# Optimization experiments

Hardware: AMD Instinct MI355X
Metric: run time of the kernel (lower is better)

The kernel has to match this reference:

```python
import jax, jax.numpy as jnp
import numpy as np

DIM = 512
HEADS = 8
HEAD_DIM = DIM // HEADS
SCALE = HEAD_DIM ** -0.5


def setup_inputs() -> dict:
    key = jax.random.key(0)
    ks = jax.random.split(key, 9)
    B, N, C = 4, 256, DIM
    w = lambda k, shape: jax.random.normal(k, shape, dtype=jnp.float32) * (shape[-1] ** -0.5)
    return {
        "q": jax.random.normal(ks[0], (B, N, C), dtype=jnp.float32),
        "k": jax.random.normal(ks[1], (B, N, C), dtype=jnp.float32),
        "v": jax.random.normal(ks[2], (B, N, C), dtype=jnp.float32),
        "relation_feature": jax.random.normal(ks[3], (B, N, N, C), dtype=jnp.float32),
        "W_q": w(ks[4], (C, C)),      # torch Linear weight: y = x @ W.T
        "W_k": w(ks[5], (C, C)),
        "W_v": w(ks[6], (C, C)),
        "W_r_conv": w(ks[7], (HEADS, C)),
        "W_r_qk": w(ks[8], (2 * C, C)),
    }


def reference(q, k, v, relation_feature, W_q, W_k, W_v, W_r_conv, W_r_qk):
    B, N1, C = q.shape
    N2 = k.shape[1]
    H, HS = HEADS, HEAD_DIM

    # project and split heads -> [B, H, N, HS]
    qh = (q @ W_q.T).reshape(B, N1, H, HS).transpose(0, 2, 1, 3)
    kh = (k @ W_k.T).reshape(B, N2, H, HS).transpose(0, 2, 1, 3)
    vh = (v @ W_v.T).reshape(B, N2, H, HS).transpose(0, 2, 1, 3)

    attn_J = jnp.einsum("bhnd,bhmd->bhnm", qh, kh)  # [B,H,N1,N2]

    # Relation-conditioned projections (computed in the original forward but
    # unused in the returned output; kept here for faithfulness of the math).
    R_qkv = (relation_feature @ W_r_qk.T).reshape(B, N1, N2, 2, H, HS)
    R_q = R_qkv[:, :, :, 0].transpose(0, 3, 1, 2, 4)  # [B,H,N1,N2,HS]
    R_k = R_qkv[:, :, :, 1].transpose(0, 3, 1, 2, 4)
    attn_R_qurt = jnp.einsum("bhnmd,bhnmd->bhnm", R_q, R_k)  # unused
    attn_R_linear = jnp.einsum("bnmc,hc->bhnm", relation_feature, W_r_conv)  # unused
    del attn_R_qurt, attn_R_linear

    attn = jax.nn.softmax(attn_J * SCALE, axis=-1)  # dropout p=0 -> identity
    x = jnp.einsum("bhnm,bhmd->bhnd", attn, vh).transpose(0, 2, 1, 3).reshape(B, N1, C)
    return (x, attn)
```

## Files before the change

kernel.cpp:

```cpp
#include <hip/hip_runtime.h>

#define HEADS 8
#define HD 64
#define NN 256
#define CC 512
#define SCALE 0.125f
#define NBLK 384
#define MAGICV 0x5F3A9C71u

typedef _Float16 half4v __attribute__((ext_vector_type(4)));
typedef _Float16 half8v __attribute__((ext_vector_type(8)));
typedef float f32x4 __attribute__((ext_vector_type(4)));

static __device__ __forceinline__ void st_agent(void* p, half4v v) {
    union { half4v h; unsigned long long u; } c;
    c.h = v;
    __hip_atomic_store((unsigned long long*)p, c.u, __ATOMIC_RELAXED,
                       __HIP_MEMORY_SCOPE_AGENT);
}

__global__ __launch_bounds__(256, 2) void fused_kernel(
    const float* __restrict__ q, const float* __restrict__ k,
    const float* __restrict__ v, const float* __restrict__ Wq,
    const float* __restrict__ Wk, const float* __restrict__ Wv,
    _Float16* __restrict__ qh, _Float16* __restrict__ kh,
    _Float16* __restrict__ vT, float* __restrict__ attn,
    float* __restrict__ x, unsigned* __restrict__ flag)
{
    __shared__ __align__(16) char smem[26624];

    const int t = threadIdx.x;
    const int lane = t & 63;
    const int blk = blockIdx.x;

    {
        _Float16 (*Xs)[72] = (_Float16 (*)[72])smem;
        _Float16 (*Ws)[72] = (_Float16 (*)[72])(smem + 9216);
        const int w = t >> 6;
        const int wr = w >> 1, wc = w & 1;
        const int l15 = lane & 15, g = lane >> 4;
        const int sc = t & 7, sr = t >> 3;

        const int z = blk >> 7;
        const int rem = blk & 127;
        const int r0 = (rem >> 3) * 64;
        const int c0 = (rem & 7) * 64;
        const float* __restrict__ X = (z == 0) ? q : (z == 1) ? k : v;
        const float* __restrict__ W = (z == 0) ? Wq : (z == 1) ? Wk : Wv;

        f32x4 acc[2][2] = {};

        for (int k0 = 0; k0 < CC; k0 += 64) {
            #pragma unroll
            for (int p = 0; p < 2; ++p) {
                int row = sr + p * 32;
                const float* gx = X + (r0 + row) * CC + k0 + sc * 8;
                const float* gw = W + (c0 + row) * CC + k0 + sc * 8;
                float4 x0 = *(const float4*)gx, x1 = *(const float4*)(gx + 4);
                float4 w0 = *(const float4*)gw, w1 = *(const float4*)(gw + 4);
                half8v hx, hw;
                hx[0] = (_Float16)x0.x; hx[1] = (_Float16)x0.y;
                hx[2] = (_Float16)x0.z; hx[3] = (_Float16)x0.w;
                hx[4] = (_Float16)x1.x; hx[5] = (_Float16)x1.y;
                hx[6] = (_Float16)x1.z; hx[7] = (_Float16)x1.w;
                hw[0] = (_Float16)w0.x; hw[1] = (_Float16)w0.y;
                hw[2] = (_Float16)w0.z; hw[3] = (_Float16)w0.w;
                hw[4] = (_Float16)w1.x; hw[5] = (_Float16)w1.y;
                hw[6] = (_Float16)w1.z; hw[7] = (_Float16)w1.w;
                *(half8v*)&Xs[row][sc * 8] = hx;
                *(half8v*)&Ws[row][sc * 8] = hw;
            }
            __syncthreads();
            #pragma unroll
            for (int kk = 0; kk < 2; ++kk) {
                half8v af[2], bf[2];
                #pragma unroll
                for (int mi = 0; mi < 2; ++mi)
                    af[mi] = *(const half8v*)((z == 2)
                        ? &Xs[wr * 32 + mi * 16 + l15][kk * 32 + g * 8]
                        : &Ws[wr * 32 + mi * 16 + l15][kk * 32 + g * 8]);
                #pragma unroll
                for (int ni = 0; ni < 2; ++ni)
                    bf[ni] = *(const half8v*)((z == 2)
                        ? &Ws[wc * 32 + ni * 16 + l15][kk * 32 + g * 8]
                        : &Xs[wc * 32 + ni * 16 + l15][kk * 32 + g * 8]);
                #pragma unroll
                for (int mi = 0; mi < 2; ++mi)
                    #pragma unroll
                    for (int ni = 0; ni < 2; ++ni)
                        acc[mi][ni] = __builtin_amdgcn_mfma_f32_16x16x32_f16(
                            af[mi], bf[ni], acc[mi][ni], 0, 0, 0);
            }
            __syncthreads();
        }

        #pragma unroll
        for (int mi = 0; mi < 2; ++mi) {
            #pragma unroll
            for (int ni = 0; ni < 2; ++ni) {
                f32x4 a = acc[mi][ni];
                half4v hv;
                hv[0] = (_Float16)a[0]; hv[1] = (_Float16)a[1];
                hv[2] = (_Float16)a[2]; hv[3] = (_Float16)a[3];
                if (z < 2) {
                    int ch  = c0 + wr * 32 + mi * 16 + g * 4;
                    int tok = r0 + wc * 32 + ni * 16 + l15;
                    int bb = tok >> 8, n = tok & 255, h = ch >> 6, d = ch & 63;
                    _Float16* dst = ((z == 0) ? qh : kh)
                                  + (((bb * HEADS + h) * NN + n) * HD + d);
                    st_agent(dst, hv);
                } else {
                    int tok = r0 + wr * 32 + mi * 16 + g * 4;
                    int ch  = c0 + wc * 32 + ni * 16 + l15;
                    int bb = tok >> 8, m = tok & 255, h = ch >> 6, d = ch & 63;
                    _Float16* dst = vT + (((bb * HEADS + h) * HD + d) * NN + m);
                    st_agent(dst, hv);
                }
            }
        }
    }

    __syncthreads();
    if (t == 0)
        __hip_atomic_store(flag + blk, MAGICV, __ATOMIC_RELAXED,
                           __HIP_MEMORY_SCOPE_AGENT);
    if (blk >= 256) return;

    {
        const int bbb = blk >> 6;
        const int hh  = (blk >> 3) & 7;
        const int nt  = blk & 7;
        if (t < 9) {
            int dep;
            if (t == 0)      dep = (bbb * 4 + (nt >> 1)) * 8 + hh;
            else if (t < 5)  dep = 128 + (bbb * 4 + (t - 1)) * 8 + hh;
            else             dep = 256 + (bbb * 4 + (t - 5)) * 8 + hh;
            while (__hip_atomic_load(flag + dep, __ATOMIC_RELAXED,
                                     __HIP_MEMORY_SCOPE_AGENT) != MAGICV)
                __builtin_amdgcn_s_sleep(2);
        }
        __syncthreads();
    }

    const int bh = blk >> 3, bb = bh >> 3, h = bh & 7;
    const int n0 = (blk & 7) * 32;
    const int w = __builtin_amdgcn_readfirstlane(t >> 6);
    const int rg = w & 1, mh = w >> 1;
    const int l15 = lane & 15, g = lane >> 4;
    const int n = n0 + rg * 16 + l15;

    _Float16 (*Plds)[16][136] = (_Float16 (*)[16][136])smem;
    float* red  = (float*)(smem + 17408);
    float* Olds = (float*)(smem + 17920);

    const _Float16* qb = qh + (bh * NN + n) * HD + g * 8;
    half8v bq0 = *(const half8v*)qb;
    half8v bq1 = *(const half8v*)(qb + 32);

    f32x4 acc[8] = {};
    const _Float16* kb = kh + (bh * NN + mh * 128 + l15) * HD + g * 8;
    #pragma unroll
    for (int nf = 0; nf < 8; ++nf) {
        half8v a0 = *(const half8v*)(kb + nf * 16 * HD);
        half8v a1 = *(const half8v*)(kb + nf * 16 * HD + 32);
        acc[nf] = __builtin_amdgcn_mfma_f32_16x16x32_f16(a0, bq0, acc[nf], 0, 0, 0);
        acc[nf] = __builtin_amdgcn_mfma_f32_16x16x32_f16(a1, bq1, acc[nf], 0, 0, 0);
    }

    float mx = -3.0e38f;
    #pragma unroll
    for (int nf = 0; nf < 8; ++nf)
        #pragma unroll
        for (int r = 0; r < 4; ++r) mx = fmaxf(mx, acc[nf][r]);
    mx = fmaxf(mx, __shfl_xor(mx, 16, 64));
    mx = fmaxf(mx, __shfl_xor(mx, 32, 64));
    const float ml = mx * SCALE;

    float sloc = 0.f;
    #pragma unroll
    for (int nf = 0; nf < 8; ++nf)
        #pragma unroll
        for (int r = 0; r < 4; ++r) {
            float e = __expf(acc[nf][r] * SCALE - ml);
            acc[nf][r] = e;
            sloc += e;
        }
    sloc += __shfl_xor(sloc, 16, 64);
    sloc += __shfl_xor(sloc, 32, 64);

    if (g == 0) {
        red[((rg * 2 + mh) * 16 + l15) * 2 + 0] = ml;
        red[((rg * 2 + mh) * 16 + l15) * 2 + 1] = sloc;
    }
    __syncthreads();
    const float mo = red[((rg * 2 + (mh ^ 1)) * 16 + l15) * 2 + 0];
    const float so = red[((rg * 2 + (mh ^ 1)) * 16 + l15) * 2 + 1];
    const float M = fmaxf(ml, mo);
    const float fl = __expf(ml - M);
    const float pscale = fl / (sloc * fl + so * __expf(mo - M));

    float* arow = attn + (bh * NN + n) * NN + mh * 128;
    #pragma unroll
    for (int nf = 0; nf < 8; ++nf) {
        float4 pv4;
        pv4.x = acc[nf][0] * pscale; pv4.y = acc[nf][1] * pscale;
        pv4.z = acc[nf][2] * pscale; pv4.w = acc[nf][3] * pscale;
        *(float4*)(arow + nf * 16 + g * 4) = pv4;
        half4v hv;
        hv[0] = (_Float16)pv4.x; hv[1] = (_Float16)pv4.y;
        hv[2] = (_Float16)pv4.z; hv[3] = (_Float16)pv4.w;
        *(half4v*)&Plds[w][l15][nf * 16 + g * 4] = hv;
    }
    asm volatile("s_waitcnt lgkmcnt(0)" ::: "memory");

    half8v pb[4];
    #pragma unroll
    for (int mt = 0; mt < 4; ++mt)
        pb[mt] = *(const half8v*)&Plds[w][l15][mt * 32 + g * 8];

    f32x4 O[4] = {};
    #pragma unroll
    for (int df = 0; df < 4; ++df) {
        const _Float16* vb = vT + (bh * HD + df * 16 + l15) * NN + mh * 128 + g * 8;
        #pragma unroll
        for (int mt = 0; mt < 4; ++mt) {
            half8v av = *(const half8v*)(vb + mt * 32);
            O[df] = __builtin_amdgcn_mfma_f32_16x16x32_f16(av, pb[mt], O[df], 0, 0, 0);
        }
    }

    if (mh == 1) {
        #pragma unroll
        for (int df = 0; df < 4; ++df)
            *(f32x4*)&Olds[(rg * 16 + l15) * 68 + df * 16 + g * 4] = O[df];
    }
    __syncthreads();
    if (mh == 0) {
        float* xb = x + (bb * NN + n) * CC + h * HD;
        #pragma unroll
        for (int df = 0; df < 4; ++df) {
            f32x4 o2 = *(const f32x4*)&Olds[(rg * 16 + l15) * 68 + df * 16 + g * 4];
            float4 st;
            st.x = O[df][0] + o2[0]; st.y = O[df][1] + o2[1];
            st.z = O[df][2] + o2[2]; st.w = O[df][3] + o2[3];
            *(float4*)(xb + df * 16 + g * 4) = st;
        }
    }
}

extern "C" void kernel_launch(void* const* d_in, const int* in_sizes, int n_in,
                              void* d_out, int out_size, void* d_ws, size_t ws_size,
                              hipStream_t stream) {
    const float* q  = (const float*)d_in[0];
    const float* k  = (const float*)d_in[1];
    const float* v  = (const float*)d_in[2];
    const float* Wq = (const float*)d_in[4];
    const float* Wk = (const float*)d_in[5];
    const float* Wv = (const float*)d_in[6];

    float* x    = (float*)d_out;
    float* attn = (float*)d_out + 4 * 256 * 512;

    _Float16* qh = (_Float16*)d_ws;
    _Float16* kh = qh + 32 * 256 * 64;
    _Float16* vT = kh + 32 * 256 * 64;
    unsigned* flag = (unsigned*)((char*)d_ws + (4u << 20));

    fused_kernel<<<dim3(NBLK), dim3(256), 0, stream>>>(
        q, k, v, Wq, Wk, Wv, qh, kh, vT, attn, x, flag);
}
```

Baseline: 25.71 us.

## Stage full B operand in LDS once and stream A fragments from global

The projection phase now loads the whole 64x512 B-operand tile into shared memory in a single pass, then removes the per-k-step LDS staging and barriers. Each wave reads its A-operand fragments straight from global memory into registers, converting to fp16 inline, with the k loop fully unrolled. The aim is to drop the 16 __syncthreads per tile and the LDS round trip for A. In exchange, LDS use grows to about 65 KB, which may reduce the 2-blocks-per-CU occupancy, and A is reloaded from global by the two waves that share a row band.

```diff
diff --git a/kernel.cpp b/kernel.cpp
--- a/kernel.cpp
+++ b/kernel.cpp
@@ -11,6 +11,15 @@
 typedef _Float16 half4v __attribute__((ext_vector_type(4)));
 typedef _Float16 half8v __attribute__((ext_vector_type(8)));
 typedef float f32x4 __attribute__((ext_vector_type(4)));
+
+static __device__ __forceinline__ half8v cvt8(float4 a, float4 b) {
+    half8v h;
+    h[0] = (_Float16)a.x; h[1] = (_Float16)a.y;
+    h[2] = (_Float16)a.z; h[3] = (_Float16)a.w;
+    h[4] = (_Float16)b.x; h[5] = (_Float16)b.y;
+    h[6] = (_Float16)b.z; h[7] = (_Float16)b.w;
+    return h;
+}
 
 static __device__ __forceinline__ void st_agent(void* p, half4v v) {
     union { half4v h; unsigned long long u; } c;
@@ -27,19 +36,17 @@
     _Float16* __restrict__ vT, float* __restrict__ attn,
     float* __restrict__ x, unsigned* __restrict__ flag)
 {
-    __shared__ __align__(16) char smem[26624];
+    __shared__ __align__(16) char smem[66560];
 
     const int t = threadIdx.x;
     const int lane = t & 63;
     const int blk = blockIdx.x;
 
     {
-        _Float16 (*Xs)[72] = (_Float16 (*)[72])smem;
-        _Float16 (*Ws)[72] = (_Float16 (*)[72])(smem + 9216);
+        _Float16 (*Bs)[520] = (_Float16 (*)[520])smem;
         const int w = t >> 6;
         const int wr = w >> 1, wc = w & 1;
         const int l15 = lane & 15, g = lane >> 4;
-        const int sc = t & 7, sr = t >> 3;
 
         const int z = blk >> 7;
         const int rem = blk & 127;
@@ -48,50 +55,48 @@
         const float* __restrict__ X = (z == 0) ? q : (z == 1) ? k : v;
         const float* __restrict__ W = (z == 0) ? Wq : (z == 1) ? Wk : Wv;
 
+        const float* bsrc = (z == 2) ? (W + c0 * CC) : (X + r0 * CC);
+        const int srow = t >> 5;
+        const int scol = (t & 31) * 16;
+        #pragma unroll
+        for (int rr = 0; rr < 8; ++rr) {
+            int row = rr * 8 + srow;
+            const float* ga = bsrc + row * CC + scol;
+            float4 a0 = *(const float4*)ga,       a1 = *(const float4*)(ga + 4);
+            float4 a2 = *(const float4*)(ga + 8), a3 = *(const float4*)(ga + 12);
+            *(half8v*)&Bs[row][scol]     = cvt8(a0, a1);
+            *(half8v*)&Bs[row][scol + 8] = cvt8(a2, a3);
+        }
+        __syncthreads();
+
+        const float* asrc = (z == 2) ? (X + r0 * CC) : (W + c0 * CC);
         f32x4 acc[2][2] = {};
 
+        #pragma unroll
         for (int k0 = 0; k0 < CC; k0 += 64) {
-            #pragma unroll
-            for (int p = 0; p < 2; ++p) {
-                int row = sr + p * 32;
-                const float* gx = X + (r0 + row) * CC + k0 + sc * 8;
-                const float* gw = W + (c0 + row) * CC + k0 + sc * 8;
-                float4 x0 = *(const float4*)gx, x1 = *(const float4*)(gx + 4);
-                float4 w0 = *(const float4*)gw, w1 = *(const float4*)(gw + 4);
-                half8v hx, hw;
-                hx[0] = (_Float16)x0.x; hx[1] = (_Float16)x0.y;
-                hx[2] = (_Float16)x0.z; hx[3] = (_Float16)x0.w;
-                hx[4] = (_Float16)x1.x; hx[5] = (_Float16)x1.y;
-                hx[6] = (_Float16)x1.z; hx[7] = (_Float16)x1.w;
-                hw[0] = (_Float16)w0.x; hw[1] = (_Float16)w0.y;
-                hw[2] = (_Float16)w0.z; hw[3] = (_Float16)w0.w;
-                hw[4] = (_Float16)w1.x; hw[5] = (_Float16)w1.y;
-                hw[6] = (_Float16)w1.z; hw[7] = (_Float16)w1.w;
-                *(half8v*)&Xs[row][sc * 8] = hx;
-                *(half8v*)&Ws[row][sc * 8] = hw;
-            }
-            __syncthreads();
-            #pragma unroll
-            for (int kk = 0; kk < 2; ++kk) {
-                half8v af[2], bf[2];
+            half8v af[2][2], bf[2][2];
+            #pragma unroll
+            for (int kk = 0; kk < 2; ++kk)
                 #pragma unroll
-                for (int mi = 0; mi < 2; ++mi)
-                    af[mi] = *(const half8v*)((z == 2)
-                        ? &Xs[wr * 32 + mi * 16 + l15][kk * 32 + g * 8]
-                        : &Ws[wr * 32 + mi * 16 + l15][kk * 32 + g * 8]);
+                for (int mi = 0; mi < 2; ++mi) {
+                    const float* ga = asrc + (wr * 32 + mi * 16 + l15) * CC
+                                    + k0 + kk * 32 + g * 8;
+                    af[kk][mi] = cvt8(*(const float4*)ga, *(const float4*)(ga + 4));
+                }
+            #pragma unroll
+            for (int kk = 0; kk < 2; ++kk)
                 #pragma unroll
                 for (int ni = 0; ni < 2; ++ni)
-                    bf[ni] = *(const half8v*)((z == 2)
-                        ? &Ws[wc * 32 + ni * 16 + l15][kk * 32 + g * 8]
-                        : &Xs[wc * 32 + ni * 16 + l15][kk * 32 + g * 8]);
+                    bf[kk][ni] = *(const half8v*)
+                        &Bs[wc * 32 + ni * 16 + l15][k0 + kk * 32 + g * 8];
+            #pragma unroll
+            for (int kk = 0; kk < 2; ++kk)
                 #pragma unroll
                 for (int mi = 0; mi < 2; ++mi)
                     #pragma unroll
                     for (int ni = 0; ni < 2; ++ni)
                         acc[mi][ni] = __builtin_amdgcn_mfma_f32_16x16x32_f16(
-                            af[mi], bf[ni], acc[mi][ni], 0, 0, 0);
-            }
-            __syncthreads();
+                            af[kk][mi], bf[kk][ni], acc[mi][ni], 0, 0, 0);
         }
 
         #pragma unroll
```

Measured after the change: 36.30 us. +41.2%, slower.

## Prefetch next K-tile into registers and remap attention block-to-head order

Applied to the files above, without the earlier changes.

The projection GEMM loop now loads the next 64-wide K slice of X and W into registers right after the shared-memory barrier, so those global loads overlap the MFMA work on the current slice instead of stalling at the top of each iteration. Separately, the attention-phase blocks are reindexed so consecutive block IDs cover different (batch, head) pairs rather than different row tiles of one head. The intent is to spread dependency waits and K/V reads across heads. The prefetch costs extra registers, which may pressure occupancy under launch_bounds(256,2).

```diff
diff --git a/kernel.cpp b/kernel.cpp
--- a/kernel.cpp
+++ b/kernel.cpp
@@ -11,6 +11,15 @@
 typedef _Float16 half4v __attribute__((ext_vector_type(4)));
 typedef _Float16 half8v __attribute__((ext_vector_type(8)));
 typedef float f32x4 __attribute__((ext_vector_type(4)));
+
+static __device__ __forceinline__ half8v cvt8(float4 a, float4 b) {
+    half8v h;
+    h[0] = (_Float16)a.x; h[1] = (_Float16)a.y;
+    h[2] = (_Float16)a.z; h[3] = (_Float16)a.w;
+    h[4] = (_Float16)b.x; h[5] = (_Float16)b.y;
+    h[6] = (_Float16)b.z; h[7] = (_Float16)b.w;
+    return h;
+}
 
 static __device__ __forceinline__ void st_agent(void* p, half4v v) {
     union { half4v h; unsigned long long u; } c;
@@ -48,29 +57,32 @@
         const float* __restrict__ X = (z == 0) ? q : (z == 1) ? k : v;
         const float* __restrict__ W = (z == 0) ? Wq : (z == 1) ? Wk : Wv;
 
+        const float* gx0 = X + (r0 + sr) * CC + sc * 8;
+        const float* gx1 = X + (r0 + sr + 32) * CC + sc * 8;
+        const float* gw0 = W + (c0 + sr) * CC + sc * 8;
+        const float* gw1 = W + (c0 + sr + 32) * CC + sc * 8;
+
+        float4 xa0 = *(const float4*)gx0, xa1 = *(const float4*)(gx0 + 4);
+        float4 xb0 = *(const float4*)gx1, xb1 = *(const float4*)(gx1 + 4);
+        float4 wa0 = *(const float4*)gw0, wa1 = *(const float4*)(gw0 + 4);
+        float4 wb0 = *(const float4*)gw1, wb1 = *(const float4*)(gw1 + 4);
+
         f32x4 acc[2][2] = {};
 
         for (int k0 = 0; k0 < CC; k0 += 64) {
-            #pragma unroll
-            for (int p = 0; p < 2; ++p) {
-                int row = sr + p * 32;
-                const float* gx = X + (r0 + row) * CC + k0 + sc * 8;
-                const float* gw = W + (c0 + row) * CC + k0 + sc * 8;
-                float4 x0 = *(const float4*)gx, x1 = *(const float4*)(gx + 4);
-                float4 w0 = *(const float4*)gw, w1 = *(const float4*)(gw + 4);
-                half8v hx, hw;
-                hx[0] = (_Float16)x0.x; hx[1] = (_Float16)x0.y;
-                hx[2] = (_Float16)x0.z; hx[3] = (_Float16)x0.w;
-                hx[4] = (_Float16)x1.x; hx[5] = (_Float16)x1.y;
-                hx[6] = (_Float16)x1.z; hx[7] = (_Float16)x1.w;
-                hw[0] = (_Float16)w0.x; hw[1] = (_Float16)w0.y;
-                hw[2] = (_Float16)w0.z; hw[3] = (_Float16)w0.w;
-                hw[4] = (_Float16)w1.x; hw[5] = (_Float16)w1.y;
-                hw[6] = (_Float16)w1.z; hw[7] = (_Float16)w1.w;
-                *(half8v*)&Xs[row][sc * 8] = hx;
-                *(half8v*)&Ws[row][sc * 8] = hw;
+            *(half8v*)&Xs[sr][sc * 8]      = cvt8(xa0, xa1);
+            *(half8v*)&Xs[sr + 32][sc * 8] = cvt8(xb0, xb1);
+            *(half8v*)&Ws[sr][sc * 8]      = cvt8(wa0, wa1);
+            *(half8v*)&Ws[sr + 32][sc * 8] = cvt8(wb0, wb1);
+            __syncthreads();
+
+            if (k0 + 64 < CC) {
+                xa0 = *(const float4*)(gx0 + k0 + 64); xa1 = *(const float4*)(gx0 + k0 + 68);
+                xb0 = *(const float4*)(gx1 + k0 + 64); xb1 = *(const float4*)(gx1 + k0 + 68);
+                wa0 = *(const float4*)(gw0 + k0 + 64); wa1 = *(const float4*)(gw0 + k0 + 68);
+                wb0 = *(const float4*)(gw1 + k0 + 64); wb1 = *(const float4*)(gw1 + k0 + 68);
             }
-            __syncthreads();
+
             #pragma unroll
             for (int kk = 0; kk < 2; ++kk) {
                 half8v af[2], bf[2];
@@ -126,15 +138,14 @@
                            __HIP_MEMORY_SCOPE_AGENT);
     if (blk >= 256) return;
 
+    const int bh = blk & 31, bb = bh >> 3, h = bh & 7;
+    const int nt = blk >> 5;
     {
-        const int bbb = blk >> 6;
-        const int hh  = (blk >> 3) & 7;
-        const int nt  = blk & 7;
         if (t < 9) {
             int dep;
-            if (t == 0)      dep = (bbb * 4 + (nt >> 1)) * 8 + hh;
-            else if (t < 5)  dep = 128 + (bbb * 4 + (t - 1)) * 8 + hh;
-            else             dep = 256 + (bbb * 4 + (t - 5)) * 8 + hh;
+            if (t == 0)      dep = (bb * 4 + (nt >> 1)) * 8 + h;
+            else if (t < 5)  dep = 128 + (bb * 4 + (t - 1)) * 8 + h;
+            else             dep = 256 + (bb * 4 + (t - 5)) * 8 + h;
             while (__hip_atomic_load(flag + dep, __ATOMIC_RELAXED,
                                      __HIP_MEMORY_SCOPE_AGENT) != MAGICV)
                 __builtin_amdgcn_s_sleep(2);
@@ -142,8 +153,7 @@
         __syncthreads();
     }
 
-    const int bh = blk >> 3, bb = bh >> 3, h = bh & 7;
-    const int n0 = (blk & 7) * 32;
+    const int n0 = nt * 32;
     const int w = __builtin_amdgcn_readfirstlane(t >> 6);
     const int rg = w & 1, mh = w >> 1;
     const int l15 = lane & 15, g = lane >> 4;
```

New measurement: 27.98 us. +8.8%, slower.
